# Kernel tuning notes

Hardware: AMD Instinct MI355X
Metric: run time of the kernel (lower is better)

## Reference

```python
import jax, jax.numpy as jnp
import numpy as np


def setup_inputs() -> dict:
    key = jax.random.key(0)
    ks = jax.random.split(key, 8)
    B, IN, H, OUT = 8192, 1024, 2048, 1024
    SIGMA_MIN, SIGMA_MAX, PHASE = 0.9, 0.999, 2.0 * np.pi
    # recurrence decay params, initialized as in the torch module
    rng = np.random.RandomState(0)
    u1 = rng.random_sample(H)
    u2 = rng.random_sample(H)
    v = -0.5 * np.log(u1 * (SIGMA_MAX ** 2 - SIGMA_MIN ** 2) + SIGMA_MIN ** 2)
    theta = u2 * PHASE
    scale_b = 1.0 / np.sqrt(IN)
    scale_c = 1.0 / np.sqrt(H)
    return {
        "x": jax.random.normal(ks[0], (B, IN), dtype=jnp.float32),
        "h_prev": jax.random.normal(ks[1], (B, H), dtype=jnp.float32),
        "Br": jax.random.normal(ks[2], (H, IN), dtype=jnp.float32) * scale_b,
        "Bi": jax.random.normal(ks[3], (H, IN), dtype=jnp.float32) * scale_b,
        "Cr": jax.random.normal(ks[4], (OUT, H), dtype=jnp.float32) * scale_c,
        "Ci": jax.random.normal(ks[5], (OUT, H), dtype=jnp.float32) * scale_c,
        "v_log": jnp.asarray(np.log(v), dtype=jnp.float32),
        "theta_log": jnp.asarray(np.log(theta), dtype=jnp.float32),
    }


def reference(x, h_prev, Br, Bi, Cr, Ci, v_log, theta_log):
    # effective diagonal recurrence weight w = exp(-exp(v_log) + i*exp(theta_log))
    mag = jnp.exp(-jnp.exp(v_log))            # [H]
    ang = jnp.exp(theta_log)                  # [H]
    wr = mag * jnp.cos(ang)
    wi = mag * jnp.sin(ang)
    # h = B(x) + h_prev * w  (h_prev is real -> imag part comes only from wi)
    # complexLinear on real x: real = x@Br^T, imag = x@Bi^T
    hr = jnp.einsum('bi,hi->bh', x, Br) + h_prev * wr   # [B,H]
    hi = jnp.einsum('bi,hi->bh', x, Bi) + h_prev * wi   # [B,H]
    # out = Re(C(h)) = hr@Cr^T - hi@Ci^T
    out = jnp.einsum('bh,oh->bo', hr, Cr) - jnp.einsum('bh,oh->bo', hi, Ci)
    return out
```

## Files before the change

### kernel.cpp

```cpp
#include <hip/hip_runtime.h>
#include <stdint.h>

typedef unsigned short u16;
typedef short bf16x8 __attribute__((ext_vector_type(8)));
typedef float f32x4 __attribute__((ext_vector_type(4)));

typedef void as1_void __attribute__((address_space(1)));
typedef void as3_void __attribute__((address_space(3)));

__device__ inline u16 f32_to_bf16(float f) {
    uint32_t u = __builtin_bit_cast(uint32_t, f);
    u += 0x7fffu + ((u >> 16) & 1u);
    return (u16)(u >> 16);
}

__device__ inline void gld_lds16(const void* g, void* l) {
    __builtin_amdgcn_global_load_lds((as1_void*)g, (as3_void*)l, 16, 0, 0);
}



__global__ void prep_kernel(const float* __restrict__ Cr, const float* __restrict__ Ci,
                            const float* __restrict__ Br, const float* __restrict__ Bi,
                            const float* __restrict__ v_log, const float* __restrict__ th_log,
                            u16* __restrict__ Ccat, u16* __restrict__ Bcat,
                            u16* __restrict__ Cwbf)
{
    __shared__ float t[32][33];
    const int b = blockIdx.x, tid = threadIdx.x;

    if (b < 4096) {
        int i = b * 256 + tid;
        int e = i * 4;
        int o = e >> 12;
        int k = e & 4095;
        float4 f; float s;
        if (k < 2048) { f = *(const float4*)(Cr + (size_t)o * 2048 + k);          s =  1.f; }
        else          { f = *(const float4*)(Ci + (size_t)o * 2048 + (k - 2048)); s = -1.f; }
        ushort4 u;
        u.x = f32_to_bf16(s * f.x); u.y = f32_to_bf16(s * f.y);
        u.z = f32_to_bf16(s * f.z); u.w = f32_to_bf16(s * f.w);
        ((ushort4*)Ccat)[i] = u;
    } else if (b < 8192) {
        int b2 = b - 4096;
        const float* src = (b2 & 2048) ? Bi : Br;
        int colOff = (b2 & 2048) ? 2048 : 0;
        int c0 = (b2 & 31) * 32, r0 = ((b2 >> 5) & 63) * 32;
        int tx = tid & 31, ty = tid >> 5;
#pragma unroll
        for (int j = 0; j < 4; j++)
            t[ty + j * 8][tx] = src[(size_t)(r0 + ty + j * 8) * 1024 + c0 + tx];
        __syncthreads();
#pragma unroll
        for (int j = 0; j < 4; j++)
            Bcat[(size_t)(c0 + ty + j * 8) * 4096 + colOff + r0 + tx] =
                f32_to_bf16(t[tx][ty + j * 8]);
    } else {
        int j = (b - 8192) * 256 + tid;
        int e = j * 4;
        int o = e >> 11;
        int h = e & 2047;
        float4 cr = *(const float4*)(Cr + (size_t)o * 2048 + h);
        float4 ci = *(const float4*)(Ci + (size_t)o * 2048 + h);
        float4 vl = *(const float4*)(v_log + h);
        float4 tl = *(const float4*)(th_log + h);
        float mag, ang, wr, wi;
        ushort4 u;
        mag = expf(-expf(vl.x)); ang = expf(tl.x); wr = mag * cosf(ang); wi = mag * sinf(ang);
        u.x = f32_to_bf16(cr.x * wr - ci.x * wi);
        mag = expf(-expf(vl.y)); ang = expf(tl.y); wr = mag * cosf(ang); wi = mag * sinf(ang);
        u.y = f32_to_bf16(cr.y * wr - ci.y * wi);
        mag = expf(-expf(vl.z)); ang = expf(tl.z); wr = mag * cosf(ang); wi = mag * sinf(ang);
        u.z = f32_to_bf16(cr.z * wr - ci.z * wi);
        mag = expf(-expf(vl.w)); ang = expf(tl.w); wr = mag * cosf(ang); wi = mag * sinf(ang);
        u.w = f32_to_bf16(cr.w * wr - ci.w * wi);
        ((ushort4*)Cwbf)[j] = u;
    }
}


__global__ void reduce_cast_kernel(const float* __restrict__ partials,
                                   const float* __restrict__ x,
                                   const float* __restrict__ h_prev,
                                   u16* __restrict__ Wmain,
                                   u16* __restrict__ x_bf,
                                   u16* __restrict__ hp_bf)
{
    const int b = blockIdx.x, tid = threadIdx.x;
    if (b < 1024) {
        int i = b * 256 + tid;
        int e = i * 4;
        float4 s = *(const float4*)(partials + e);
#pragma unroll
        for (int z = 1; z < 8; z++) {
            float4 p = *(const float4*)(partials + ((size_t)z << 20) + e);
            s.x += p.x; s.y += p.y; s.z += p.z; s.w += p.w;
        }
        ushort4 u;
        u.x = f32_to_bf16(s.x); u.y = f32_to_bf16(s.y);
        u.z = f32_to_bf16(s.z); u.w = f32_to_bf16(s.w);
        ((ushort4*)Wmain)[i] = u;
    } else if (b < 9216) {
        int i = (b - 1024) * 256 + tid;
        float4 f = ((const float4*)x)[i];
        ushort4 o;
        o.x = f32_to_bf16(f.x); o.y = f32_to_bf16(f.y);
        o.z = f32_to_bf16(f.z); o.w = f32_to_bf16(f.w);
        ((ushort4*)x_bf)[i] = o;
    } else {
        int i = (b - 9216) * 256 + tid;
        float4 f = ((const float4*)h_prev)[i];
        ushort4 o;
        o.x = f32_to_bf16(f.x); o.y = f32_to_bf16(f.y);
        o.z = f32_to_bf16(f.z); o.w = f32_to_bf16(f.w);
        ((ushort4*)hp_bf)[i] = o;
    }
}


__global__ void reduce_only_kernel(const float* __restrict__ partials,
                                   u16* __restrict__ Wmain) {
    int i = blockIdx.x * blockDim.x + threadIdx.x;
    int e = i * 4;
    float4 s = *(const float4*)(partials + e);
#pragma unroll
    for (int z = 1; z < 8; z++) {
        float4 p = *(const float4*)(partials + ((size_t)z << 20) + e);
        s.x += p.x; s.y += p.y; s.z += p.z; s.w += p.w;
    }
    ushort4 u;
    u.x = f32_to_bf16(s.x); u.y = f32_to_bf16(s.y);
    u.z = f32_to_bf16(s.z); u.w = f32_to_bf16(s.w);
    ((ushort4*)Wmain)[i] = u;
}

__global__ void cast_both_kernel(const float* __restrict__ x,
                                 const float* __restrict__ h_prev,
                                 u16* __restrict__ dst) {
    const int n4x = 8192 * 1024 / 4;
    int i = blockIdx.x * blockDim.x + threadIdx.x;
    float4 f = (i < n4x) ? ((const float4*)x)[i] : ((const float4*)h_prev)[i - n4x];
    ushort4 o;
    o.x = f32_to_bf16(f.x); o.y = f32_to_bf16(f.y);
    o.z = f32_to_bf16(f.z); o.w = f32_to_bf16(f.w);
    ((ushort4*)dst)[i] = o;
}


__global__ __launch_bounds__(256)
void gemm_splitk_kernel(const u16* __restrict__ A, const u16* __restrict__ B,
                        float* __restrict__ partials)
{
    __shared__ __align__(16) u16 ldsA[128 * 64];
    __shared__ __align__(16) u16 ldsB[128 * 64];
    const int K = 4096;

    const int tid = threadIdx.x, wid = tid >> 6, lane = tid & 63;
    const int quad = lane >> 4, l16 = lane & 15;
    const int wm = wid >> 1, wn = wid & 1;
    const int bm = blockIdx.y, bn = blockIdx.x, bz = blockIdx.z;
    const int kb = bz * 512;

    const u16* gA[4]; const u16* gB[4];
    u16 *lA[4], *lB[4];
#pragma unroll
    for (int t = 0; t < 4; t++) {
        int s = wid * 256 + t * 64 + lane;
        int sr = s >> 3;
        int sj = (s & 7) ^ (sr & 7);
        lA[t] = ldsA + s * 8;
        lB[t] = ldsB + s * 8;
        gA[t] = A + (size_t)(bm * 128 + sr) * K + sj * 8 + kb;
        gB[t] = B + (size_t)(bn * 128 + sr) * K + sj * 8 + kb;
    }

    const f32x4 fz = {0.f, 0.f, 0.f, 0.f};
    f32x4 acc[4][4];
#pragma unroll
    for (int i = 0; i < 4; i++)
#pragma unroll
        for (int j = 0; j < 4; j++) acc[i][j] = fz;

    for (int k0 = 0; k0 < 512; k0 += 64) {
        __syncthreads();
#pragma unroll
        for (int t = 0; t < 4; t++) {
            gld_lds16(gA[t] + k0, lA[t]);
            gld_lds16(gB[t] + k0, lB[t]);
        }
        __syncthreads();
#pragma unroll
        for (int ks = 0; ks < 2; ks++) {
            bf16x8 af[4], bfr[4];
#pragma unroll
            for (int i = 0; i < 4; i++) {
                int r = wm * 64 + i * 16 + l16;
                af[i] = *(const bf16x8*)(ldsA + (r * 8 + ((ks * 4 + quad) ^ (r & 7))) * 8);
            }
#pragma unroll
            for (int j = 0; j < 4; j++) {
                int r = wn * 64 + j * 16 + l16;
                bfr[j] = *(const bf16x8*)(ldsB + (r * 8 + ((ks * 4 + quad) ^ (r & 7))) * 8);
            }
#pragma unroll
            for (int i = 0; i < 4; i++)
#pragma unroll
                for (int j = 0; j < 4; j++)
                    acc[i][j] = __builtin_amdgcn_mfma_f32_16x16x32_bf16(af[i], bfr[j], acc[i][j], 0, 0, 0);
        }
    }

    float* P = partials + ((size_t)bz << 20);
    const int gm = bm * 128 + wm * 64, gn = bn * 128 + wn * 64;
#pragma unroll
    for (int i = 0; i < 4; i++)
#pragma unroll
        for (int j = 0; j < 4; j++) {
            int col = gn + j * 16 + l16;
#pragma unroll
            for (int r = 0; r < 4; r++)
                P[(size_t)(gm + i * 16 + quad * 4 + r) * 1024 + col] = acc[i][j][r];
        }
}


__global__ __launch_bounds__(256)
void gemm_main_kernel(const u16* __restrict__ Axb, const u16* __restrict__ Ahb,
                      const u16* __restrict__ Bw,  const u16* __restrict__ Bcw,
                      float* __restrict__ out)
{
    __shared__ __align__(16) u16 ldsA[128 * 64];
    __shared__ __align__(16) u16 ldsB[128 * 64];

    const int tid = threadIdx.x, wid = tid >> 6, lane = tid & 63;
    const int quad = lane >> 4, l16 = lane & 15;
    const int wm = wid >> 1, wn = wid & 1;
    const int id = blockIdx.x;
    const int bm = id & 63, bn = id >> 6;

    int srow[4], sj[4];
    u16 *lA[4], *lB[4];
#pragma unroll
    for (int t = 0; t < 4; t++) {
        int s = wid * 256 + t * 64 + lane;
        srow[t] = s >> 3;
        sj[t] = (s & 7) ^ (srow[t] & 7);
        lA[t] = ldsA + s * 8;
        lB[t] = ldsB + s * 8;
    }

    const f32x4 fz = {0.f, 0.f, 0.f, 0.f};
    f32x4 acc[4][4];
#pragma unroll
    for (int i = 0; i < 4; i++)
#pragma unroll
        for (int j = 0; j < 4; j++) acc[i][j] = fz;

#pragma unroll 1
    for (int phase = 0; phase < 2; phase++) {
        const u16* Ap = phase ? Ahb : Axb;
        const u16* Bp = phase ? Bcw : Bw;
        const int KS = phase ? 2048 : 1024;
        const u16* gA[4]; const u16* gB[4];
#pragma unroll
        for (int t = 0; t < 4; t++) {
            gA[t] = Ap + (size_t)(bm * 128 + srow[t]) * KS + sj[t] * 8;
            gB[t] = Bp + (size_t)(bn * 128 + srow[t]) * KS + sj[t] * 8;
        }
        for (int k0 = 0; k0 < KS; k0 += 64) {
            __syncthreads();
#pragma unroll
            for (int t = 0; t < 4; t++) {
                gld_lds16(gA[t] + k0, lA[t]);
                gld_lds16(gB[t] + k0, lB[t]);
            }
            __syncthreads();
#pragma unroll
            for (int ks = 0; ks < 2; ks++) {
                bf16x8 af[4], bfr[4];
#pragma unroll
                for (int i = 0; i < 4; i++) {
                    int r = wm * 64 + i * 16 + l16;
                    af[i] = *(const bf16x8*)(ldsA + (r * 8 + ((ks * 4 + quad) ^ (r & 7))) * 8);
                }
#pragma unroll
                for (int j = 0; j < 4; j++) {
                    int r = wn * 64 + j * 16 + l16;
                    bfr[j] = *(const bf16x8*)(ldsB + (r * 8 + ((ks * 4 + quad) ^ (r & 7))) * 8);
                }
#pragma unroll
                for (int i = 0; i < 4; i++)
#pragma unroll
                    for (int j = 0; j < 4; j++)
                        acc[i][j] = __builtin_amdgcn_mfma_f32_16x16x32_bf16(af[i], bfr[j], acc[i][j], 0, 0, 0);
            }
        }
    }

    const int gm = bm * 128 + wm * 64, gn = bn * 128 + wn * 64;
#pragma unroll
    for (int i = 0; i < 4; i++)
#pragma unroll
        for (int j = 0; j < 4; j++) {
            int col = gn + j * 16 + l16;
#pragma unroll
            for (int r = 0; r < 4; r++)
                out[(size_t)(gm + i * 16 + quad * 4 + r) * 1024 + col] = acc[i][j][r];
        }
}


extern "C" void kernel_launch(void* const* d_in, const int* in_sizes, int n_in,
                              void* d_out, int out_size, void* d_ws, size_t ws_size,
                              hipStream_t stream)
{
    const float* x      = (const float*)d_in[0];
    const float* h_prev = (const float*)d_in[1];
    const float* Br     = (const float*)d_in[2];
    const float* Bi     = (const float*)d_in[3];
    const float* Cr     = (const float*)d_in[4];
    const float* Ci     = (const float*)d_in[5];
    const float* v_log  = (const float*)d_in[6];
    const float* th_log = (const float*)d_in[7];
    float* out = (float*)d_out;

    const size_t MB = 1024 * 1024;
    if (ws_size < 54 * MB) return;
    const bool big = (ws_size >= 86 * MB);

    char* ws = (char*)d_ws;
    u16*   Ccat     = (u16*)ws;
    u16*   Bcat     = (u16*)(ws + 8 * MB);
    float* partials = (float*)(ws + 16 * MB);
    u16*   x_bf     = (u16*)ws;
    u16*   Wmain    = (u16*)(ws + 48 * MB);
    u16*   Cwbf     = (u16*)(ws + 50 * MB);
    u16*   hp_bf    = big ? (u16*)(ws + 54 * MB) : (u16*)(ws + 16 * MB);

    prep_kernel<<<10240, 256, 0, stream>>>(Cr, Ci, Br, Bi, v_log, th_log,
                                           Ccat, Bcat, Cwbf);
    gemm_splitk_kernel<<<dim3(8, 8, 8), 256, 0, stream>>>(Ccat, Bcat, partials);
    if (big) {
        reduce_cast_kernel<<<25600, 256, 0, stream>>>(partials, x, h_prev,
                                                      Wmain, x_bf, hp_bf);
    } else {
        reduce_only_kernel<<<1024, 256, 0, stream>>>(partials, Wmain);
        cast_both_kernel<<<24576, 256, 0, stream>>>(x, h_prev, x_bf);
    }
    gemm_main_kernel<<<512, 256, 0, stream>>>(x_bf, hp_bf, Wmain, Cwbf, out);
}
```

Measured before the change: 246.2 us.

## Triple-buffer main GEMM LDS with async prefetch and 256x128 tiles

Rewrites the main GEMM as a 512-thread block computing a 256x128 output tile with a three-stage LDS ring buffer. Global-to-LDS loads for the next tiles are issued ahead of compute, and a vmcnt wait plus barrier replaces the two syncthreads per k-step. MFMA sections also get raised wave priority. This aims to hide memory latency and cut synchronization, at the cost of 144KB of LDS per block and half as many blocks (256) for the CUs.

```diff
diff --git a/kernel.cpp b/kernel.cpp
--- a/kernel.cpp
+++ b/kernel.cpp
@@ -224,30 +224,36 @@
 }
 
 
-__global__ __launch_bounds__(256)
+__global__ __launch_bounds__(512)
 void gemm_main_kernel(const u16* __restrict__ Axb, const u16* __restrict__ Ahb,
                       const u16* __restrict__ Bw,  const u16* __restrict__ Bcw,
                       float* __restrict__ out)
 {
-    __shared__ __align__(16) u16 ldsA[128 * 64];
-    __shared__ __align__(16) u16 ldsB[128 * 64];
+    __shared__ __align__(16) u16 lds[3][24576];
 
     const int tid = threadIdx.x, wid = tid >> 6, lane = tid & 63;
     const int quad = lane >> 4, l16 = lane & 15;
     const int wm = wid >> 1, wn = wid & 1;
     const int id = blockIdx.x;
-    const int bm = id & 63, bn = id >> 6;
-
-    int srow[4], sj[4];
-    u16 *lA[4], *lB[4];
-#pragma unroll
-    for (int t = 0; t < 4; t++) {
-        int s = wid * 256 + t * 64 + lane;
-        srow[t] = s >> 3;
-        sj[t] = (s & 7) ^ (srow[t] & 7);
-        lA[t] = ldsA + s * 8;
-        lB[t] = ldsB + s * 8;
-    }
+    const int bm = id & 31, bn = id >> 5;
+
+    int srA[4], sjA[4], srB[2], sjB[2];
+#pragma unroll
+    for (int q = 0; q < 4; q++) {
+        int s = q * 512 + tid;
+        srA[q] = s >> 3;
+        sjA[q] = (s & 7) ^ (srA[q] & 7);
+    }
+#pragma unroll
+    for (int q = 0; q < 2; q++) {
+        int s = q * 512 + tid;
+        srB[q] = s >> 3;
+        sjB[q] = (s & 7) ^ (srB[q] & 7);
+    }
+
+    u16* buf0 = &lds[0][0];
+    u16* buf1 = &lds[1][0];
+    u16* buf2 = &lds[2][0];
 
     const f32x4 fz = {0.f, 0.f, 0.f, 0.f};
     f32x4 acc[4][4];
@@ -256,48 +262,65 @@
 #pragma unroll
         for (int j = 0; j < 4; j++) acc[i][j] = fz;
 
+    auto stage = [&](int tt, u16* buf) {
+        const u16* Ab; const u16* Bb; int KS, koff;
+        if (tt < 16) { Ab = Axb; Bb = Bw;  KS = 1024; koff = tt * 64; }
+        else         { Ab = Ahb; Bb = Bcw; KS = 2048; koff = (tt - 16) * 64; }
+#pragma unroll
+        for (int q = 0; q < 4; q++)
+            gld_lds16(Ab + (size_t)(bm * 256 + srA[q]) * KS + koff + sjA[q] * 8,
+                      buf + (q * 512 + tid) * 8);
+#pragma unroll
+        for (int q = 0; q < 2; q++)
+            gld_lds16(Bb + (size_t)(bn * 128 + srB[q]) * KS + koff + sjB[q] * 8,
+                      buf + 16384 + (q * 512 + tid) * 8);
+    };
+
+    auto compute = [&](const u16* buf) {
+#pragma unroll
+        for (int ks = 0; ks < 2; ks++) {
+            bf16x8 af[4], bfr[4];
+#pragma unroll
+            for (int i = 0; i < 4; i++) {
+                int r = wm * 64 + i * 16 + l16;
+                af[i] = *(const bf16x8*)(buf + (r * 8 + ((ks * 4 + quad) ^ (r & 7))) * 8);
+            }
+#pragma unroll
+            for (int j = 0; j < 4; j++) {
+                int r = wn * 64 + j * 16 + l16;
+                bfr[j] = *(const bf16x8*)(buf + 16384 + (r * 8 + ((ks * 4 + quad) ^ (r & 7))) * 8);
+            }
+            __builtin_amdgcn_s_setprio(1);
+#pragma unroll
+            for (int i = 0; i < 4; i++)
+#pragma unroll
+                for (int j = 0; j < 4; j++)
+                    acc[i][j] = __builtin_amdgcn_mfma_f32_16x16x32_bf16(af[i], bfr[j], acc[i][j], 0, 0, 0);
+            __builtin_amdgcn_s_setprio(0);
+        }
+    };
+
+#define PUBLISH(N)                                          \
+    asm volatile("s_waitcnt vmcnt(" #N ")" ::: "memory");   \
+    __builtin_amdgcn_s_barrier();                           \
+    asm volatile("" ::: "memory")
+
+    stage(0, buf0);
+    stage(1, buf1);
+    PUBLISH(6);
+
 #pragma unroll 1
-    for (int phase = 0; phase < 2; phase++) {
-        const u16* Ap = phase ? Ahb : Axb;
-        const u16* Bp = phase ? Bcw : Bw;
-        const int KS = phase ? 2048 : 1024;
-        const u16* gA[4]; const u16* gB[4];
-#pragma unroll
-        for (int t = 0; t < 4; t++) {
-            gA[t] = Ap + (size_t)(bm * 128 + srow[t]) * KS + sj[t] * 8;
-            gB[t] = Bp + (size_t)(bn * 128 + srow[t]) * KS + sj[t] * 8;
-        }
-        for (int k0 = 0; k0 < KS; k0 += 64) {
-            __syncthreads();
-#pragma unroll
-            for (int t = 0; t < 4; t++) {
-                gld_lds16(gA[t] + k0, lA[t]);
-                gld_lds16(gB[t] + k0, lB[t]);
-            }
-            __syncthreads();
-#pragma unroll
-            for (int ks = 0; ks < 2; ks++) {
-                bf16x8 af[4], bfr[4];
-#pragma unroll
-                for (int i = 0; i < 4; i++) {
-                    int r = wm * 64 + i * 16 + l16;
-                    af[i] = *(const bf16x8*)(ldsA + (r * 8 + ((ks * 4 + quad) ^ (r & 7))) * 8);
-                }
-#pragma unroll
-                for (int j = 0; j < 4; j++) {
-                    int r = wn * 64 + j * 16 + l16;
-                    bfr[j] = *(const bf16x8*)(ldsB + (r * 8 + ((ks * 4 + quad) ^ (r & 7))) * 8);
-                }
-#pragma unroll
-                for (int i = 0; i < 4; i++)
-#pragma unroll
-                    for (int j = 0; j < 4; j++)
-                        acc[i][j] = __builtin_amdgcn_mfma_f32_16x16x32_bf16(af[i], bfr[j], acc[i][j], 0, 0, 0);
-            }
-        }
-    }
-
-    const int gm = bm * 128 + wm * 64, gn = bn * 128 + wn * 64;
+    for (int it = 0; it < 15; it++) {
+        stage(3 * it + 2, buf2); compute(buf0); PUBLISH(6);
+        stage(3 * it + 3, buf0); compute(buf1); PUBLISH(6);
+        stage(3 * it + 4, buf1); compute(buf2); PUBLISH(6);
+    }
+    stage(47, buf2); compute(buf0); PUBLISH(6);
+    compute(buf1); PUBLISH(0);
+    compute(buf2);
+#undef PUBLISH
+
+    const int gm = bm * 256 + wm * 64, gn = bn * 128 + wn * 64;
 #pragma unroll
     for (int i = 0; i < 4; i++)
 #pragma unroll
@@ -347,5 +370,5 @@
         reduce_only_kernel<<<1024, 256, 0, stream>>>(partials, Wmain);
         cast_both_kernel<<<24576, 256, 0, stream>>>(x, h_prev, x_bf);
     }
-    gemm_main_kernel<<<512, 256, 0, stream>>>(x_bf, hp_bf, Wmain, Cwbf, out);
-}
+    gemm_main_kernel<<<256, 512, 0, stream>>>(x_bf, hp_bf, Wmain, Cwbf, out);
+}
```

Result: no change. 246.2 us (-0.0%).
